# Kernel optimization log

Hardware: AMD Instinct MI355X
Metric: run time of the kernel (lower is better)

The kernel has to match this reference:

```python
import jax, jax.numpy as jnp
import numpy as np

L, S, D, H, DL, V, B = 8, 1024, 768, 12, 64, 512, 8
NB, NM = 32, 64  # big_bird neighbours, global memory columns


def _bigbird_mask():
    i = np.arange(S)[:, None]
    j = np.arange(S)[None, :]
    m = ((np.abs(i - j) <= NB) | (j < NM)) & (j <= i)  # window + global cols, then tril
    return jnp.asarray(m)[None, None]  # [1,1,S,S]


def _ln(x, g, b):
    mu = x.mean(-1, keepdims=True)
    var = ((x - mu) ** 2).mean(-1, keepdims=True)
    return (x - mu) / jnp.sqrt(var + 1e-5) * g + b


def setup_inputs() -> dict:
    key = jax.random.key(0)
    ks = jax.random.split(key, 16)
    s = 0.02
    d = {
        'x': jax.random.randint(ks[0], (B, S), 0, V),
        'targets': jax.random.randint(ks[1], (B, S), 0, V),
        'wte': jax.random.normal(ks[2], (V, D), jnp.float32) * s,
        'pos': jnp.zeros((1, S, D), jnp.float32),
        'ln1_g': jnp.ones((L, D)), 'ln1_b': jnp.zeros((L, D)),
        'wq': jax.random.normal(ks[3], (L, D, D)) * s, 'bq': jnp.zeros((L, D)),
        'wk': jax.random.normal(ks[4], (L, D, D)) * s, 'bk': jnp.zeros((L, D)),
        'wv': jax.random.normal(ks[5], (L, D, D)) * s, 'bv': jnp.zeros((L, D)),
        'ln2_g': jnp.ones((L, D)), 'ln2_b': jnp.zeros((L, D)),
        'w1': jax.random.normal(ks[6], (L, D, 4 * D)) * s, 'b1': jnp.zeros((L, 4 * D)),
        'w2': jax.random.normal(ks[7], (L, 4 * D, D)) * s, 'b2': jnp.zeros((L, D)),
        'lnf_g': jnp.ones((D,)), 'lnf_b': jnp.zeros((D,)),
        'w_out': jax.random.normal(ks[8], (D, V)) * s,
    }
    return d


def _forward(x, targets, wte, pos, ln1_g, ln1_b, wq, bq, wk, bk, wv, bv,
             ln2_g, ln2_b, w1, b1, w2, b2, lnf_g, lnf_b, w_out):
    mask = _bigbird_mask()
    h = wte[x] + pos  # [B,S,D]
    scale = DL ** -0.5
    neg_inf = jnp.array(float('-inf'), h.dtype)
    for l in range(L):
        a = _ln(h, ln1_g[l], ln1_b[l])
        q = (a @ wq[l] + bq[l]).reshape(B, S, H, DL).transpose(0, 2, 1, 3)
        k = (a @ wk[l] + bk[l]).reshape(B, S, H, DL).transpose(0, 2, 1, 3)
        v = (a @ wv[l] + bv[l]).reshape(B, S, H, DL).transpose(0, 2, 1, 3)
        att = jnp.einsum('bhqd,bhkd->bhqk', q, k) * scale
        att = jnp.where(mask, att, neg_inf)
        att = jax.nn.softmax(att, axis=-1)
        z = jnp.einsum('bhqk,bhkd->bhqd', att, v)
        z = z.transpose(0, 2, 1, 3).reshape(B, S, D)
        h = h + z  # note: W_0 is defined in the torch module but never applied
        m = _ln(h, ln2_g[l], ln2_b[l])
        h = h + jax.nn.gelu(m @ w1[l] + b1[l], approximate=False) @ w2[l] + b2[l]
    h = _ln(h, lnf_g, lnf_b)
    pred = h @ w_out  # [B,S,V]
    logp = jax.nn.log_softmax(pred.reshape(B * S, V), axis=-1)
    loss = -jnp.take_along_axis(logp, targets.reshape(-1, 1), axis=1).mean()
    return pred, loss


def reference(x, targets, wte, pos, ln1_g, ln1_b, wq, bq, wk, bk, wv, bv,
              ln2_g, ln2_b, w1, b1, w2, b2, lnf_g, lnf_b, w_out):
    return _forward(x, targets, wte, pos, ln1_g, ln1_b, wq, bq, wk, bk, wv, bv,
                    ln2_g, ln2_b, w1, b1, w2, b2, lnf_g, lnf_b, w_out)
```

## Files before the change

kernel.cpp:

```cpp
#include <hip/hip_runtime.h>
#include <hip/hip_bf16.h>

#define DEV __device__ __forceinline__

typedef __attribute__((ext_vector_type(8))) short short8;
typedef __attribute__((ext_vector_type(4))) float f32x4;

DEV unsigned short f2bf(float f){
  unsigned int u = __builtin_bit_cast(unsigned int, f);
  u += 0x7FFFu + ((u >> 16) & 1u);
  return (unsigned short)(u >> 16);
}

DEV void gld_lds16(const void* g, void* l){
  __builtin_amdgcn_global_load_lds((const __attribute__((address_space(1))) void*)g,
                                   (__attribute__((address_space(3))) void*)l, 16, 0, 0);
}

__global__ void k_embed(const int* __restrict__ x, const float* __restrict__ wte,
                        const float* __restrict__ pos, float* __restrict__ h){
  int i = blockIdx.x * 256 + threadIdx.x;
  int row = i / 768, d = i - row * 768;
  int s = row & 1023;
  h[i] = wte[x[row] * 768 + d] + pos[s * 768 + d];
}

__global__ void k_ln(const float* __restrict__ src, const float* __restrict__ g,
                     const float* __restrict__ b, unsigned short* __restrict__ out){
  int row = blockIdx.x, t = threadIdx.x;
  const float* p = src + (size_t)row * 768;
  float v0 = p[t], v1 = p[t + 256], v2 = p[t + 512];
  float s = v0 + v1 + v2;
  float sq = v0 * v0 + v1 * v1 + v2 * v2;
  #pragma unroll
  for(int m = 32; m >= 1; m >>= 1){ s += __shfl_xor(s, m); sq += __shfl_xor(sq, m); }
  __shared__ float red[8];
  int w = t >> 6;
  if((t & 63) == 0){ red[w] = s; red[4 + w] = sq; }
  __syncthreads();
  float S  = red[0] + red[1] + red[2] + red[3];
  float SQ = red[4] + red[5] + red[6] + red[7];
  float mu  = S * (1.0f / 768.0f);
  float var = SQ * (1.0f / 768.0f) - mu * mu;
  float inv = rsqrtf(var + 1e-5f);
  unsigned short* o = out + (size_t)row * 768;
  o[t]       = f2bf((v0 - mu) * inv * g[t]       + b[t]);
  o[t + 256] = f2bf((v1 - mu) * inv * g[t + 256] + b[t + 256]);
  o[t + 512] = f2bf((v2 - mu) * inv * g[t + 512] + b[t + 512]);
}

DEV void tr_tile64(float (*tl)[33], const float* __restrict__ src, unsigned short* __restrict__ dst,
                   int R, int C, int tx, int ty, int tid){
  int lx = tid & 31, ly = tid >> 5;
  int r0 = ty * 64, c0 = tx * 32;
  #pragma unroll
  for(int i = 0; i < 8; i++)
    tl[ly + 8 * i][lx] = src[(size_t)(r0 + ly + 8 * i) * C + (c0 + lx)];
  __syncthreads();
  #pragma unroll
  for(int j = 0; j < 4; j++){
    int oc = ly + 8 * j;
    unsigned int pk = (unsigned int)f2bf(tl[2 * lx][oc]) |
                      ((unsigned int)f2bf(tl[2 * lx + 1][oc]) << 16);
    *(unsigned int*)(dst + (size_t)(c0 + oc) * R + r0 + 2 * lx) = pk;
  }
}

__global__ void k_convert_all(const float* __restrict__ wq, const float* __restrict__ wk,
                              const float* __restrict__ wv, const float* __restrict__ w1,
                              const float* __restrict__ w2, const float* __restrict__ bq,
                              const float* __restrict__ bk, const float* __restrict__ bv,
                              unsigned short* __restrict__ wall, float* __restrict__ qkvb,
                              int l0){
  __shared__ float tl[64][33];
  int l = l0 + blockIdx.y, slot = blockIdx.y;
  int bid = blockIdx.x, tid = threadIdx.x;
  unsigned short* wqkv_t = wall + (size_t)slot * 6488064;
  unsigned short* w1_t   = wqkv_t + 1769472;
  unsigned short* w2_t   = w1_t + 2359296;
  float* qb = qkvb + slot * 2304;
  const float* wq_l = wq + (size_t)l * 589824;
  const float* wk_l = wk + (size_t)l * 589824;
  const float* wv_l = wv + (size_t)l * 589824;
  const float* w1_l = w1 + (size_t)l * 2359296;
  const float* w2_l = w2 + (size_t)l * 2359296;
  if(bid < 864){
    int which = bid / 288, t = bid - which * 288;
    const float* src = which == 0 ? wq_l : which == 1 ? wk_l : wv_l;
    tr_tile64(tl, src, wqkv_t + (size_t)which * 589824, 768, 768, t % 24, t / 24, tid);
  } else if(bid < 864 + 1152){
    int t = bid - 864;
    tr_tile64(tl, w1_l, w1_t, 768, 3072, t % 96, t / 96, tid);
  } else if(bid < 864 + 2304){
    int t = bid - 2016;
    tr_tile64(tl, w2_l, w2_t, 3072, 768, t % 24, t / 24, tid);
  } else {
    for(int i = tid; i < 768; i += 256){
      qb[i] = bq[l * 768 + i]; qb[768 + i] = bk[l * 768 + i]; qb[1536 + i] = bv[l * 768 + i];
    }
  }
}

__global__ void k_transpose(const float* __restrict__ src, unsigned short* __restrict__ dst,
                            int R, int C){
  __shared__ float tl[64][33];
  int nx = C / 32;
  tr_tile64(tl, src, dst, R, C, blockIdx.x % nx, blockIdx.x / nx, threadIdx.x);
}

template<int EPI, int MW, int NB>
__global__ __launch_bounds__(MW * 128, 4)
void k_gemm(const unsigned short* __restrict__ A, const unsigned short* __restrict__ Bt,
            const float* __restrict__ bias, int K,
            float* __restrict__ fout, unsigned short* __restrict__ o0,
            unsigned short* __restrict__ o1, unsigned short* __restrict__ o2){
  constexpr int THREADS = MW * 128;
  constexpr int AL = 4;
  constexpr int BL = (2 * NB) / MW;
  __shared__ unsigned short As[MW * 64 * 64];
  __shared__ unsigned short Bs[NB * 32 * 64];
  int tid = threadIdx.x, w = tid >> 6, lane = tid & 63;
  int l15 = lane & 15, l4 = lane >> 4;
  int nbx = gridDim.x;
  int bid = blockIdx.y * nbx + blockIdx.x;
  int cpx = (nbx * gridDim.y) >> 3;
  int sid = (bid & 7) * cpx + (bid >> 3);
  int bm = sid / nbx, bn = sid - bm * nbx;
  int N = nbx * NB * 32;
  int wr = w >> 1, wc = w & 1;
  f32x4 acc[4][NB] = {};
  int rowA[AL], colA[AL], rowB[BL], colB[BL];
  #pragma unroll
  for(int i = 0; i < AL; i++){
    int o = i * THREADS * 16 + tid * 16;
    int r = o >> 7, ch = (o >> 4) & 7;
    rowA[i] = r; colA[i] = ((ch ^ (r & 7)) << 3);
  }
  #pragma unroll
  for(int i = 0; i < BL; i++){
    int o = i * THREADS * 16 + tid * 16;
    int r = o >> 7, ch = (o >> 4) & 7;
    rowB[i] = r; colB[i] = ((ch ^ (r & 7)) << 3);
  }
  const size_t aBase = (size_t)bm * (MW * 64);
  const size_t bBase = (size_t)bn * (NB * 32);
  for(int kt = 0; kt < K; kt += 64){
    #pragma unroll
    for(int i = 0; i < AL; i++)
      gld_lds16(A + (aBase + rowA[i]) * K + kt + colA[i],
                (char*)As + i * THREADS * 16 + tid * 16);
    #pragma unroll
    for(int i = 0; i < BL; i++)
      gld_lds16(Bt + (bBase + rowB[i]) * K + kt + colB[i],
                (char*)Bs + i * THREADS * 16 + tid * 16);
    __syncthreads();
    #pragma unroll
    for(int s = 0; s < 2; s++){
      short8 af[4], bfr[NB];
      #pragma unroll
      for(int m = 0; m < 4; m++){
        int r = wr * 64 + m * 16 + l15;
        int ch = s * 4 + l4;
        af[m] = *(const short8*)(As + r * 64 + ((ch ^ (r & 7)) << 3));
      }
      #pragma unroll
      for(int n = 0; n < NB; n++){
        int r = wc * (NB * 16) + n * 16 + l15;
        int ch = s * 4 + l4;
        bfr[n] = *(const short8*)(Bs + r * 64 + ((ch ^ (r & 7)) << 3));
      }
      #pragma unroll
      for(int m = 0; m < 4; m++)
        #pragma unroll
        for(int n = 0; n < NB; n++)
          acc[m][n] = __builtin_amdgcn_mfma_f32_16x16x32_bf16(af[m], bfr[n], acc[m][n], 0, 0, 0);
    }
    __syncthreads();
  }
  int r0 = bm * (MW * 64) + wr * 64 + (l4 << 2);
  int c0 = bn * (NB * 32) + wc * (NB * 16) + l15;
  if(EPI == 0){
    unsigned short* dstn[NB];
    float bvn[NB];
    #pragma unroll
    for(int n = 0; n < NB; n++){
      int col = c0 + n * 16;
      bvn[n] = bias[col];
      int which = col / 768, cc = col - which * 768;
      int hd = cc >> 6, dl = cc & 63;
      unsigned short* dst = which == 0 ? o0 : which == 1 ? o1 : o2;
      dstn[n] = dst + (size_t)hd * 65536 + dl;
    }
    #pragma unroll
    for(int m = 0; m < 4; m++){
      #pragma unroll
      for(int j = 0; j < 4; j++){
        int row = r0 + m * 16 + j;
        int bb = row >> 10, sp = row & 1023;
        size_t ro = ((size_t)bb * 12288 + sp) * 64;
        #pragma unroll
        for(int n = 0; n < NB; n++)
          dstn[n][ro] = f2bf(acc[m][n][j] + bvn[n]);
      }
    }
  } else {
    float bvn[NB];
    #pragma unroll
    for(int n = 0; n < NB; n++) bvn[n] = (EPI == 3) ? 0.0f : bias[c0 + n * 16];
    #pragma unroll
    for(int m = 0; m < 4; m++){
      #pragma unroll
      for(int j = 0; j < 4; j++){
        int row = r0 + m * 16 + j;
        #pragma unroll
        for(int n = 0; n < NB; n++){
          int col = c0 + n * 16;
          float v = acc[m][n][j] + bvn[n];
          if(EPI == 1){
            float t = v * (1.5957691f + 0.07135481f * v * v);
            float gl = v * __builtin_amdgcn_rcpf(1.0f + __expf(-t));
            o0[(size_t)row * N + col] = f2bf(gl);
          } else if(EPI == 2){
            fout[(size_t)row * 768 + col] += v;
          } else {
            fout[(size_t)row * 512 + col] = v;
          }
        }
      }
    }
  }
}

__global__ __launch_bounds__(256)
void k_attn(const unsigned short* __restrict__ qg, const unsigned short* __restrict__ kg,
            const unsigned short* __restrict__ vg, float* __restrict__ h){
  __shared__ unsigned short Vt[64 * 256];
  __shared__ unsigned short Ps[4][32 * 128];
  int qb = blockIdx.x, bh = blockIdx.y;
  int tid = threadIdx.x, w = tid >> 6, lane = tid & 63;
  int b = bh / 12, hd = bh - b * 12;
  int wbase = qb * 128 - 32;
  const unsigned short* vb = vg + (size_t)bh * 1024 * 64;
  for(int u = tid; u < 224 * 8; u += 256){
    int slot = u >> 3, c8 = u & 7;
    int j = slot < 64 ? slot : wbase + (slot - 64);
    if(j < 0) j = 0;
    short8 vv = *(const short8*)(vb + (size_t)j * 64 + c8 * 8);
    #pragma unroll
    for(int e = 0; e < 8; e++){
      int d = c8 * 8 + e;
      Vt[d * 256 + (((slot >> 3) ^ (d & 7)) << 3) + (slot & 7)] = (unsigned short)vv[e];
    }
  }
  __syncthreads();
  int i0 = qb * 128 + 32 * w;
  const unsigned short* qrow = qg + (size_t)bh * 1024 * 64;
  const unsigned short* krow = kg + (size_t)bh * 1024 * 64;
  short8 qf[2][2];
  #pragma unroll
  for(int m = 0; m < 2; m++)
    #pragma unroll
    for(int s = 0; s < 2; s++)
      qf[m][s] = *(const short8*)(qrow + (size_t)(i0 + m * 16 + (lane & 15)) * 64 + s * 32 + ((lane >> 4) << 3));
  f32x4 sacc[2][8] = {};
  #pragma unroll
  for(int n = 0; n < 8; n++){
    int jk = (n < 4) ? (n * 16 + (lane & 15))
                     : (wbase + 32 * w + (n - 4) * 16 + (lane & 15));
    int jc = jk < 0 ? 0 : jk;
    const unsigned short* kr = krow + (size_t)jc * 64 + ((lane >> 4) << 3);
    short8 k0 = *(const short8*)(kr);
    short8 k1 = *(const short8*)(kr + 32);
    #pragma unroll
    for(int m = 0; m < 2; m++){
      sacc[m][n] = __builtin_amdgcn_mfma_f32_16x16x32_bf16(qf[m][0], k0, sacc[m][n], 0, 0, 0);
      sacc[m][n] = __builtin_amdgcn_mfma_f32_16x16x32_bf16(qf[m][1], k1, sacc[m][n], 0, 0, 0);
    }
  }
  #pragma unroll
  for(int m = 0; m < 2; m++)
    #pragma unroll
    for(int n = 0; n < 8; n++){
      int s_ = n * 16 + (lane & 15);
      int jkey = (n < 4) ? s_ : (wbase + 32 * w + (s_ - 64));
      #pragma unroll
      for(int j = 0; j < 4; j++){
        int qi = i0 + m * 16 + ((lane >> 4) << 2) + j;
        bool ok = (n < 4) ? (jkey <= qi)
                          : (jkey >= 64 && jkey <= qi && (qi - jkey) <= 32);
        sacc[m][n][j] = ok ? sacc[m][n][j] * 0.125f : -1e30f;
      }
    }
  float rsum[2][4];
  #pragma unroll
  for(int m = 0; m < 2; m++)
    #pragma unroll
    for(int j = 0; j < 4; j++){
      float mx = sacc[m][0][j];
      #pragma unroll
      for(int n = 1; n < 8; n++) mx = fmaxf(mx, sacc[m][n][j]);
      mx = fmaxf(mx, __shfl_xor(mx, 1)); mx = fmaxf(mx, __shfl_xor(mx, 2));
      mx = fmaxf(mx, __shfl_xor(mx, 4)); mx = fmaxf(mx, __shfl_xor(mx, 8));
      float sm = 0.f;
      #pragma unroll
      for(int n = 0; n < 8; n++){
        float e = expf(sacc[m][n][j] - mx);
        sacc[m][n][j] = e;
        sm += e;
      }
      sm += __shfl_xor(sm, 1); sm += __shfl_xor(sm, 2);
      sm += __shfl_xor(sm, 4); sm += __shfl_xor(sm, 8);
      rsum[m][j] = sm;
    }
  unsigned short* Pw = Ps[w];
  #pragma unroll
  for(int m = 0; m < 2; m++)
    #pragma unroll
    for(int n = 0; n < 8; n++){
      int s_ = n * 16 + (lane & 15);
      #pragma unroll
      for(int j = 0; j < 4; j++){
        int ql = m * 16 + ((lane >> 4) << 2) + j;
        Pw[ql * 128 + (((s_ >> 3) ^ (ql & 7)) << 3) + (s_ & 7)] = f2bf(sacc[m][n][j]);
      }
    }
  f32x4 oacc[2][4] = {};
  #pragma unroll
  for(int s = 0; s < 4; s++){
    short8 pa[2];
    #pragma unroll
    for(int m = 0; m < 2; m++){
      int ql = m * 16 + (lane & 15);
      int ch = s * 4 + (lane >> 4);
      pa[m] = *(const short8*)(Pw + ql * 128 + ((ch ^ (ql & 7)) << 3));
    }
    int kk = s * 32 + ((lane >> 4) << 3);
    int slot0 = kk < 64 ? kk : 64 + 32 * w + (kk - 64);
    #pragma unroll
    for(int n = 0; n < 4; n++){
      int d = n * 16 + (lane & 15);
      short8 vv = *(const short8*)(Vt + d * 256 + (((slot0 >> 3) ^ (d & 7)) << 3));
      #pragma unroll
      for(int m = 0; m < 2; m++)
        oacc[m][n] = __builtin_amdgcn_mfma_f32_16x16x32_bf16(pa[m], vv, oacc[m][n], 0, 0, 0);
    }
  }
  #pragma unroll
  for(int m = 0; m < 2; m++)
    #pragma unroll
    for(int j = 0; j < 4; j++){
      int ql = m * 16 + ((lane >> 4) << 2) + j;
      float inv = 1.0f / rsum[m][j];
      size_t base = ((size_t)(b * 1024 + i0 + ql)) * 768 + hd * 64;
      #pragma unroll
      for(int n = 0; n < 4; n++){
        int d = n * 16 + (lane & 15);
        h[base + d] += oacc[m][n][j] * inv;
      }
    }
}

__global__ void k_rowloss(const float* __restrict__ pred, const int* __restrict__ tgt,
                          float* __restrict__ rowloss){
  int row = blockIdx.x * 4 + (threadIdx.x >> 6);
  int lane = threadIdx.x & 63;
  const float* p = pred + (size_t)row * 512 + lane * 8;
  float v[8];
  #pragma unroll
  for(int i = 0; i < 8; i++) v[i] = p[i];
  float mx = v[0];
  #pragma unroll
  for(int i = 1; i < 8; i++) mx = fmaxf(mx, v[i]);
  #pragma unroll
  for(int m = 1; m < 64; m <<= 1) mx = fmaxf(mx, __shfl_xor(mx, m));
  float se = 0.f;
  #pragma unroll
  for(int i = 0; i < 8; i++) se += expf(v[i] - mx);
  #pragma unroll
  for(int m = 1; m < 64; m <<= 1) se += __shfl_xor(se, m);
  int t = tgt[row];
  float pt = 0.f;
  int base = lane * 8;
  #pragma unroll
  for(int i = 0; i < 8; i++) pt = (t == base + i) ? v[i] : pt;
  #pragma unroll
  for(int m = 1; m < 64; m <<= 1) pt += __shfl_xor(pt, m);
  if(lane == 0) rowloss[row] = -(pt - mx - logf(se));
}

__global__ void k_lossfinal(const float* __restrict__ rowloss, float* __restrict__ out){
  int tid = threadIdx.x;
  float s = 0.f;
  for(int i = tid; i < 8192; i += 256) s += rowloss[i];
  #pragma unroll
  for(int m = 32; m >= 1; m >>= 1) s += __shfl_xor(s, m);
  __shared__ float red[4];
  if((tid & 63) == 0) red[tid >> 6] = s;
  __syncthreads();
  if(tid == 0) out[0] = (red[0] + red[1] + red[2] + red[3]) * (1.0f / 8192.0f);
}

extern "C" void kernel_launch(void* const* d_in, const int* in_sizes, int n_in,
                              void* d_out, int out_size, void* d_ws, size_t ws_size,
                              hipStream_t stream){
  const int*   x       = (const int*)d_in[0];
  const int*   targets = (const int*)d_in[1];
  const float* wte     = (const float*)d_in[2];
  const float* pos     = (const float*)d_in[3];
  const float* ln1_g   = (const float*)d_in[4];
  const float* ln1_b   = (const float*)d_in[5];
  const float* wq      = (const float*)d_in[6];
  const float* bq      = (const float*)d_in[7];
  const float* wk      = (const float*)d_in[8];
  const float* bk      = (const float*)d_in[9];
  const float* wv      = (const float*)d_in[10];
  const float* bv      = (const float*)d_in[11];
  const float* ln2_g   = (const float*)d_in[12];
  const float* ln2_b   = (const float*)d_in[13];
  const float* w1      = (const float*)d_in[14];
  const float* b1      = (const float*)d_in[15];
  const float* w2      = (const float*)d_in[16];
  const float* b2      = (const float*)d_in[17];
  const float* lnf_g   = (const float*)d_in[18];
  const float* lnf_b   = (const float*)d_in[19];
  const float* w_out   = (const float*)d_in[20];
  float* out = (float*)d_out;

  char* ws = (char*)d_ws;
  float*          h      = (float*)ws;
  unsigned short* a_bf   = (unsigned short*)(ws + 25165824);
  char*           big    = ws + 37748736;
  unsigned short* qbf    = (unsigned short*)big;
  unsigned short* kbf    = (unsigned short*)(big + 12582912);
  unsigned short* vbf    = (unsigned short*)(big + 25165824);
  unsigned short* tbf    = (unsigned short*)big;
  bool mega = ws_size >= 192782336ull;
  unsigned short* wall   = (unsigned short*)(ws + 88080384);
  size_t wend = 88080384ull + (mega ? 103809024ull : 12976128ull);
  unsigned short* wout_t = (unsigned short*)(ws + wend);
  float*          qkvb   = (float*)(ws + wend + 786432);
  float*          rowls  = (float*)(ws + wend + 786432 + (mega ? 73728 : 9216));

  if(mega)
    k_convert_all<<<dim3(3169, 8), 256, 0, stream>>>(wq, wk, wv, w1, w2, bq, bk, bv,
                                                     wall, qkvb, 0);
  k_transpose<<<192, 256, 0, stream>>>(w_out, wout_t, 768, 512);
  k_embed<<<24576, 256, 0, stream>>>(x, wte, pos, h);
  for(int l = 0; l < 8; l++){
    if(!mega)
      k_convert_all<<<dim3(3169, 1), 256, 0, stream>>>(wq, wk, wv, w1, w2, bq, bk, bv,
                                                       wall, qkvb, l);
    int slot = mega ? l : 0;
    unsigned short* wqkv_l = wall + (size_t)slot * 6488064;
    unsigned short* w1_l   = wqkv_l + 1769472;
    unsigned short* w2_l   = w1_l + 2359296;
    float*          qkvb_l = qkvb + slot * 2304;
    k_ln<<<8192, 256, 0, stream>>>(h, ln1_g + l * 768, ln1_b + l * 768, a_bf);
    k_gemm<0,4,4><<<dim3(18, 32), 512, 0, stream>>>(a_bf, wqkv_l, qkvb_l, 768, nullptr, qbf, kbf, vbf);
    k_attn<<<dim3(8, 96), 256, 0, stream>>>(qbf, kbf, vbf, h);
    k_ln<<<8192, 256, 0, stream>>>(h, ln2_g + l * 768, ln2_b + l * 768, a_bf);
    k_gemm<1,4,4><<<dim3(24, 32), 512, 0, stream>>>(a_bf, w1_l, b1 + l * 3072, 768, nullptr, tbf, nullptr, nullptr);
    k_gemm<2,2,2><<<dim3(12, 64), 256, 0, stream>>>(tbf, w2_l, b2 + l * 768, 3072, h, nullptr, nullptr, nullptr);
  }
  k_ln<<<8192, 256, 0, stream>>>(h, lnf_g, lnf_b, a_bf);
  k_gemm<3,2,2><<<dim3(8, 64), 256, 0, stream>>>(a_bf, wout_t, nullptr, 768, out, nullptr, nullptr, nullptr);
  k_rowloss<<<2048, 256, 0, stream>>>(out, targets, rowls);
  k_lossfinal<<<1, 256, 0, stream>>>(rowls, out + 4194304);
}
```

Measured before the change: 1.595 ms.

## Double-buffer GEMM LDS tiles, shrink QKV/W1 block tiles, widen weight transpose tiles

The GEMM kernel now keeps two LDS buffers for the A and B tiles. It issues the global-to-LDS loads for the next K step before running the MFMAs on the current step, so memory latency can overlap with compute. The QKV and W1 GEMMs move from 4-wave 256-row tiles to 2-wave 128-row tiles, launched on twice as many blocks. The weight-transpose helper now handles 128x32 tiles and writes 64-bit packed bf16 stores, so the convert and transpose kernels launch half as many blocks. Doubling the LDS footprint may reduce the number of resident blocks per CU. The new transpose load pattern (16 consecutive floats per thread) may coalesce worse.

```diff
diff --git a/kernel.cpp b/kernel.cpp
--- a/kernel.cpp
+++ b/kernel.cpp
@@ -49,20 +49,24 @@
   o[t + 512] = f2bf((v2 - mu) * inv * g[t + 512] + b[t + 512]);
 }
 
-DEV void tr_tile64(float (*tl)[33], const float* __restrict__ src, unsigned short* __restrict__ dst,
-                   int R, int C, int tx, int ty, int tid){
+DEV void tr_tile128(float (*tl)[33], const float* __restrict__ src, unsigned short* __restrict__ dst,
+                    int R, int C, int tx, int ty, int tid){
+  int r0 = ty * 128, c0 = tx * 32;
+  int lr = tid >> 1, lc = (tid & 1) * 16;
+  const float* sp = src + (size_t)(r0 + lr) * C + c0 + lc;
+  #pragma unroll
+  for(int e = 0; e < 16; e++) tl[lr][lc + e] = sp[e];
+  __syncthreads();
   int lx = tid & 31, ly = tid >> 5;
-  int r0 = ty * 64, c0 = tx * 32;
-  #pragma unroll
-  for(int i = 0; i < 8; i++)
-    tl[ly + 8 * i][lx] = src[(size_t)(r0 + ly + 8 * i) * C + (c0 + lx)];
-  __syncthreads();
   #pragma unroll
   for(int j = 0; j < 4; j++){
     int oc = ly + 8 * j;
-    unsigned int pk = (unsigned int)f2bf(tl[2 * lx][oc]) |
-                      ((unsigned int)f2bf(tl[2 * lx + 1][oc]) << 16);
-    *(unsigned int*)(dst + (size_t)(c0 + oc) * R + r0 + 2 * lx) = pk;
+    unsigned long long pk =
+        (unsigned long long)f2bf(tl[4 * lx][oc]) |
+        ((unsigned long long)f2bf(tl[4 * lx + 1][oc]) << 16) |
+        ((unsigned long long)f2bf(tl[4 * lx + 2][oc]) << 32) |
+        ((unsigned long long)f2bf(tl[4 * lx + 3][oc]) << 48);
+    *(unsigned long long*)(dst + (size_t)(c0 + oc) * R + r0 + 4 * lx) = pk;
   }
 }
 
@@ -72,7 +76,7 @@
                               const float* __restrict__ bk, const float* __restrict__ bv,
                               unsigned short* __restrict__ wall, float* __restrict__ qkvb,
                               int l0){
-  __shared__ float tl[64][33];
+  __shared__ float tl[128][33];
   int l = l0 + blockIdx.y, slot = blockIdx.y;
   int bid = blockIdx.x, tid = threadIdx.x;
   unsigned short* wqkv_t = wall + (size_t)slot * 6488064;
@@ -84,16 +88,16 @@
   const float* wv_l = wv + (size_t)l * 589824;
   const float* w1_l = w1 + (size_t)l * 2359296;
   const float* w2_l = w2 + (size_t)l * 2359296;
-  if(bid < 864){
-    int which = bid / 288, t = bid - which * 288;
+  if(bid < 432){
+    int which = bid / 144, t = bid - which * 144;
     const float* src = which == 0 ? wq_l : which == 1 ? wk_l : wv_l;
-    tr_tile64(tl, src, wqkv_t + (size_t)which * 589824, 768, 768, t % 24, t / 24, tid);
-  } else if(bid < 864 + 1152){
-    int t = bid - 864;
-    tr_tile64(tl, w1_l, w1_t, 768, 3072, t % 96, t / 96, tid);
-  } else if(bid < 864 + 2304){
-    int t = bid - 2016;
-    tr_tile64(tl, w2_l, w2_t, 3072, 768, t % 24, t / 24, tid);
+    tr_tile128(tl, src, wqkv_t + (size_t)which * 589824, 768, 768, t % 24, t / 24, tid);
+  } else if(bid < 432 + 576){
+    int t = bid - 432;
+    tr_tile128(tl, w1_l, w1_t, 768, 3072, t % 96, t / 96, tid);
+  } else if(bid < 432 + 1152){
+    int t = bid - 1008;
+    tr_tile128(tl, w2_l, w2_t, 3072, 768, t % 24, t / 24, tid);
   } else {
     for(int i = tid; i < 768; i += 256){
       qb[i] = bq[l * 768 + i]; qb[768 + i] = bk[l * 768 + i]; qb[1536 + i] = bv[l * 768 + i];
@@ -103,9 +107,9 @@
 
 __global__ void k_transpose(const float* __restrict__ src, unsigned short* __restrict__ dst,
                             int R, int C){
-  __shared__ float tl[64][33];
+  __shared__ float tl[128][33];
   int nx = C / 32;
-  tr_tile64(tl, src, dst, R, C, blockIdx.x % nx, blockIdx.x / nx, threadIdx.x);
+  tr_tile128(tl, src, dst, R, C, blockIdx.x % nx, blockIdx.x / nx, threadIdx.x);
 }
 
 template<int EPI, int MW, int NB>
@@ -117,8 +121,8 @@
   constexpr int THREADS = MW * 128;
   constexpr int AL = 4;
   constexpr int BL = (2 * NB) / MW;
-  __shared__ unsigned short As[MW * 64 * 64];
-  __shared__ unsigned short Bs[NB * 32 * 64];
+  __shared__ unsigned short As[2][MW * 64 * 64];
+  __shared__ unsigned short Bs[2][NB * 32 * 64];
   int tid = threadIdx.x, w = tid >> 6, lane = tid & 63;
   int l15 = lane & 15, l4 = lane >> 4;
   int nbx = gridDim.x;
@@ -144,16 +148,28 @@
   }
   const size_t aBase = (size_t)bm * (MW * 64);
   const size_t bBase = (size_t)bn * (NB * 32);
-  for(int kt = 0; kt < K; kt += 64){
-    #pragma unroll
-    for(int i = 0; i < AL; i++)
-      gld_lds16(A + (aBase + rowA[i]) * K + kt + colA[i],
-                (char*)As + i * THREADS * 16 + tid * 16);
-    #pragma unroll
-    for(int i = 0; i < BL; i++)
-      gld_lds16(Bt + (bBase + rowB[i]) * K + kt + colB[i],
-                (char*)Bs + i * THREADS * 16 + tid * 16);
-    __syncthreads();
+  #pragma unroll
+  for(int i = 0; i < AL; i++)
+    gld_lds16(A + (aBase + rowA[i]) * K + colA[i], (char*)As[0] + i * THREADS * 16 + tid * 16);
+  #pragma unroll
+  for(int i = 0; i < BL; i++)
+    gld_lds16(Bt + (bBase + rowB[i]) * K + colB[i], (char*)Bs[0] + i * THREADS * 16 + tid * 16);
+  __syncthreads();
+  int cur = 0;
+  for(int kt = 0; kt < K; kt += 64, cur ^= 1){
+    if(kt + 64 < K){
+      int kn = kt + 64;
+      #pragma unroll
+      for(int i = 0; i < AL; i++)
+        gld_lds16(A + (aBase + rowA[i]) * K + kn + colA[i],
+                  (char*)As[cur ^ 1] + i * THREADS * 16 + tid * 16);
+      #pragma unroll
+      for(int i = 0; i < BL; i++)
+        gld_lds16(Bt + (bBase + rowB[i]) * K + kn + colB[i],
+                  (char*)Bs[cur ^ 1] + i * THREADS * 16 + tid * 16);
+    }
+    const unsigned short* Ac = As[cur];
+    const unsigned short* Bc = Bs[cur];
     #pragma unroll
     for(int s = 0; s < 2; s++){
       short8 af[4], bfr[NB];
@@ -161,13 +177,13 @@
       for(int m = 0; m < 4; m++){
         int r = wr * 64 + m * 16 + l15;
         int ch = s * 4 + l4;
-        af[m] = *(const short8*)(As + r * 64 + ((ch ^ (r & 7)) << 3));
+        af[m] = *(const short8*)(Ac + r * 64 + ((ch ^ (r & 7)) << 3));
       }
       #pragma unroll
       for(int n = 0; n < NB; n++){
         int r = wc * (NB * 16) + n * 16 + l15;
         int ch = s * 4 + l4;
-        bfr[n] = *(const short8*)(Bs + r * 64 + ((ch ^ (r & 7)) << 3));
+        bfr[n] = *(const short8*)(Bc + r * 64 + ((ch ^ (r & 7)) << 3));
       }
       #pragma unroll
       for(int m = 0; m < 4; m++)
@@ -442,13 +458,13 @@
   float*          rowls  = (float*)(ws + wend + 786432 + (mega ? 73728 : 9216));
 
   if(mega)
-    k_convert_all<<<dim3(3169, 8), 256, 0, stream>>>(wq, wk, wv, w1, w2, bq, bk, bv,
+    k_convert_all<<<dim3(1585, 8), 256, 0, stream>>>(wq, wk, wv, w1, w2, bq, bk, bv,
                                                      wall, qkvb, 0);
-  k_transpose<<<192, 256, 0, stream>>>(w_out, wout_t, 768, 512);
+  k_transpose<<<96, 256, 0, stream>>>(w_out, wout_t, 768, 512);
   k_embed<<<24576, 256, 0, stream>>>(x, wte, pos, h);
   for(int l = 0; l < 8; l++){
     if(!mega)
-      k_convert_all<<<dim3(3169, 1), 256, 0, stream>>>(wq, wk, wv, w1, w2, bq, bk, bv,
+      k_convert_all<<<dim3(1585, 1), 256, 0, stream>>>(wq, wk, wv, w1, w2, bq, bk, bv,
                                                        wall, qkvb, l);
     int slot = mega ? l : 0;
     unsigned short* wqkv_l = wall + (size_t)slot * 6488064;
@@ -456,10 +472,10 @@
     unsigned short* w2_l   = w1_l + 2359296;
     float*          qkvb_l = qkvb + slot * 2304;
     k_ln<<<8192, 256, 0, stream>>>(h, ln1_g + l * 768, ln1_b + l * 768, a_bf);
-    k_gemm<0,4,4><<<dim3(18, 32), 512, 0, stream>>>(a_bf, wqkv_l, qkvb_l, 768, nullptr, qbf, kbf, vbf);
+    k_gemm<0,2,4><<<dim3(18, 64), 256, 0, stream>>>(a_bf, wqkv_l, qkvb_l, 768, nullptr, qbf, kbf, vbf);
     k_attn<<<dim3(8, 96), 256, 0, stream>>>(qbf, kbf, vbf, h);
     k_ln<<<8192, 256, 0, stream>>>(h, ln2_g + l * 768, ln2_b + l * 768, a_bf);
-    k_gemm<1,4,4><<<dim3(24, 32), 512, 0, stream>>>(a_bf, w1_l, b1 + l * 3072, 768, nullptr, tbf, nullptr, nullptr);
+    k_gemm<1,2,4><<<dim3(24, 64), 256, 0, stream>>>(a_bf, w1_l, b1 + l * 3072, 768, nullptr, tbf, nullptr, nullptr);
     k_gemm<2,2,2><<<dim3(12, 64), 256, 0, stream>>>(tbf, w2_l, b2 + l * 768, 3072, h, nullptr, nullptr, nullptr);
   }
   k_ln<<<8192, 256, 0, stream>>>(h, lnf_g, lnf_b, a_bf);
```

New measurement: 1.690 ms. +6.0%, slower.
